# Optimization experiments

Hardware: AMD Instinct MI355X
Metric: run time of the kernel (lower is better)

Reference implementation:

```python
import jax, jax.numpy as jnp
import numpy as np

B, S, D, H = 4, 2048, 512, 8
HD = D // H  # head dim = 64


def setup_inputs() -> dict:
    key = jax.random.key(0)
    ks = jax.random.split(key, 7)
    s = 0.02
    return {
        "X": jax.random.normal(ks[0], (B, S, D), dtype=jnp.float32),
        "Y": jax.random.normal(ks[1], (B, S, D), dtype=jnp.float32),
        "Z": jax.random.normal(ks[2], (B, S, D), dtype=jnp.float32),
        # weights stored as [in, out] (torch Linear weight transposed)
        "Wq": jax.random.normal(ks[3], (D, D), dtype=jnp.float32) * s,
        "Wk": jax.random.normal(ks[4], (D, D), dtype=jnp.float32) * s,
        "Wv": jax.random.normal(ks[5], (D, D), dtype=jnp.float32) * s,  # dead in original forward
        "Wo": jax.random.normal(ks[6], (D, D), dtype=jnp.float32) * s,
    }


def _split_heads(t):
    # [B, S, D] -> [B, H, S, HD]
    return t.reshape(B, S, H, HD).transpose(0, 2, 1, 3)


def reference(X, Y, Z, Wq, Wk, Wv, Wo):
    q = _split_heads(X @ Wq)
    k = _split_heads(Y @ Wk)
    # NOTE: original module (faithfully) uses W_o for the value projection; W_v is unused.
    v = _split_heads(Z @ Wo)
    scores = jnp.einsum("bhqd,bhkd->bhqk", q, k) / jnp.sqrt(jnp.float32(HD))
    # sigmoid(s) > 0.5  <=>  s > 0 (sigmoid strictly monotone); keep score else 0
    scores = jnp.where(scores > 0, scores, jnp.float32(0))
    attn = jax.nn.softmax(scores, axis=-1)
    out = jnp.einsum("bhqk,bhkd->bhqd", attn, v)  # dropout inactive at eval
    out = out.transpose(0, 2, 1, 3).reshape(B, S, D)  # merge heads
    return out @ Wo
```

## Files before the change

kernel.cpp:

```cpp
#include <hip/hip_runtime.h>
#include <math.h>

#define S_LEN 2048
#define DIM   512
#define M_TOT 8192
#define NCH   (S_LEN / 64)

typedef __attribute__((ext_vector_type(8))) short bf16x8;
typedef __attribute__((ext_vector_type(4))) short bf16x4;
typedef __attribute__((ext_vector_type(4))) float f32x4;
typedef __attribute__((ext_vector_type(16))) float f32x16;

#define MFMA(a, b, c)   __builtin_amdgcn_mfma_f32_16x16x32_bf16((a), (b), (c), 0, 0, 0)
#define MFMA32(a, b, c) __builtin_amdgcn_mfma_f32_32x32x16_bf16((a), (b), (c), 0, 0, 0)

#define QSCALE 0.18033688011112042f

__device__ __forceinline__ short f2b(float x) {
    union { float f; unsigned u; } v; v.f = x;
    unsigned r = v.u + 0x7FFFu + ((v.u >> 16) & 1u);
    return (short)(r >> 16);
}

__device__ __forceinline__ unsigned cvtpk(float a, float b) {
    unsigned r;
    asm("v_cvt_pk_bf16_f32 %0, %1, %2" : "=v"(r) : "v"(a), "v"(b));
    return r;
}

__device__ __forceinline__ bf16x8 cvt8(float4 lo, float4 hi) {
    union { unsigned u[4]; bf16x8 v; } o;
    o.u[0] = cvtpk(lo.x, lo.y);
    o.u[1] = cvtpk(lo.z, lo.w);
    o.u[2] = cvtpk(hi.x, hi.y);
    o.u[3] = cvtpk(hi.z, hi.w);
    return o.v;
}

__device__ __forceinline__ float fast_exp2(float x) {
#if __has_builtin(__builtin_amdgcn_exp2f)
    return __builtin_amdgcn_exp2f(x);
#else
    return __expf(x * 0.693147180559945f);
#endif
}

__global__ __launch_bounds__(256) void prep_wt(const float* Wq, const float* Wk, const float* Wo,
                                               short* Wtq, short* Wtk, short* Wto) {
    const int zi = blockIdx.z;
    const float* W = zi == 0 ? Wq : zi == 1 ? Wk : Wo;
    short*      Wt = zi == 0 ? Wtq : zi == 1 ? Wtk : Wto;
    const float sc = zi == 0 ? QSCALE : 1.0f;
    __shared__ short Ts[64 * 72];
    const int t = threadIdx.x;
    const int k0 = blockIdx.x * 64, n0 = blockIdx.y * 64;
    #pragma unroll
    for (int it = 0; it < 4; ++it) {
        const int r = (t >> 4) + 16 * it;
        const int cq = t & 15;
        float4 v = *(const float4*)&W[(size_t)(k0 + r) * DIM + n0 + cq * 4];
        Ts[(4 * cq + 0) * 72 + r] = f2b(v.x * sc);
        Ts[(4 * cq + 1) * 72 + r] = f2b(v.y * sc);
        Ts[(4 * cq + 2) * 72 + r] = f2b(v.z * sc);
        Ts[(4 * cq + 3) * 72 + r] = f2b(v.w * sc);
    }
    __syncthreads();
    #pragma unroll
    for (int it = 0; it < 2; ++it) {
        const int n = (t >> 3) + 32 * it;
        const int sg = t & 7;
        *(bf16x8*)&Wt[(size_t)(n0 + n) * DIM + k0 + sg * 8] = *(const bf16x8*)&Ts[n * 72 + sg * 8];
    }
}

__global__ __launch_bounds__(256) void proj_gemm(const float* __restrict__ X,
                                                 const float* __restrict__ Y,
                                                 const float* __restrict__ Z,
                                                 const short* __restrict__ Wtq,
                                                 const short* __restrict__ Wtk,
                                                 const short* __restrict__ Wto,
                                                 short* __restrict__ Qb,
                                                 short* __restrict__ Kb,
                                                 short* __restrict__ Vt) {
    const int zi = blockIdx.z;
    const float* A  = zi == 0 ? X : zi == 1 ? Y : Z;
    const short* Bw = zi == 0 ? Wtq : zi == 1 ? Wtk : Wto;

    __shared__ short As[2][128 * 40];
    __shared__ short Bs[2][128 * 40];
    const int tid = threadIdx.x;
    const int w = tid >> 6, ln = tid & 63, l15 = ln & 15, quad = ln >> 4;
    const int m0 = blockIdx.x * 128, n0 = blockIdx.y * 128;
    const int wm = (w & 1) * 64, wn = (w >> 1) * 64;

    const int r0 = tid >> 2, r1 = r0 + 64;
    const int sg = tid & 3;
    const float* ap0 = A  + (size_t)(m0 + r0) * DIM + sg * 8;
    const float* ap1 = A  + (size_t)(m0 + r1) * DIM + sg * 8;
    const short* bp0 = Bw + (size_t)(n0 + r0) * DIM + sg * 8;
    const short* bp1 = Bw + (size_t)(n0 + r1) * DIM + sg * 8;

    float4 a0l, a0h, a1l, a1h;
    bf16x8 b0, b1;

    a0l = *(const float4*)ap0; a0h = *(const float4*)(ap0 + 4);
    a1l = *(const float4*)ap1; a1h = *(const float4*)(ap1 + 4);
    b0 = *(const bf16x8*)bp0;  b1 = *(const bf16x8*)bp1;
    *(bf16x8*)&As[0][r0 * 40 + sg * 8] = cvt8(a0l, a0h);
    *(bf16x8*)&As[0][r1 * 40 + sg * 8] = cvt8(a1l, a1h);
    *(bf16x8*)&Bs[0][r0 * 40 + sg * 8] = b0;
    *(bf16x8*)&Bs[0][r1 * 40 + sg * 8] = b1;
    a0l = *(const float4*)(ap0 + 32); a0h = *(const float4*)(ap0 + 36);
    a1l = *(const float4*)(ap1 + 32); a1h = *(const float4*)(ap1 + 36);
    b0 = *(const bf16x8*)(bp0 + 32);  b1 = *(const bf16x8*)(bp1 + 32);
    __syncthreads();

    f32x4 acc[4][4] = {};

    for (int k0 = 0; k0 < DIM; k0 += 32) {
        const int cur = (k0 >> 5) & 1;
        if (k0 + 32 < DIM) {
            *(bf16x8*)&As[cur ^ 1][r0 * 40 + sg * 8] = cvt8(a0l, a0h);
            *(bf16x8*)&As[cur ^ 1][r1 * 40 + sg * 8] = cvt8(a1l, a1h);
            *(bf16x8*)&Bs[cur ^ 1][r0 * 40 + sg * 8] = b0;
            *(bf16x8*)&Bs[cur ^ 1][r1 * 40 + sg * 8] = b1;
        }
        if (k0 + 64 < DIM) {
            const int kn = k0 + 64;
            a0l = *(const float4*)(ap0 + kn); a0h = *(const float4*)(ap0 + kn + 4);
            a1l = *(const float4*)(ap1 + kn); a1h = *(const float4*)(ap1 + kn + 4);
            b0 = *(const bf16x8*)(bp0 + kn);  b1 = *(const bf16x8*)(bp1 + kn);
        }

        bf16x8 af[4], bf[4];
        #pragma unroll
        for (int mf = 0; mf < 4; ++mf) af[mf] = *(const bf16x8*)&As[cur][(wm + 16 * mf + l15) * 40 + quad * 8];
        #pragma unroll
        for (int nf = 0; nf < 4; ++nf) bf[nf] = *(const bf16x8*)&Bs[cur][(wn + 16 * nf + l15) * 40 + quad * 8];
        #pragma unroll
        for (int mf = 0; mf < 4; ++mf)
            #pragma unroll
            for (int nf = 0; nf < 4; ++nf)
                acc[mf][nf] = MFMA(af[mf], bf[nf], acc[mf][nf]);
        __syncthreads();
    }

    if (zi < 2) {
        short* C = zi == 0 ? Qb : Kb;
        #pragma unroll
        for (int mf = 0; mf < 4; ++mf)
            #pragma unroll
            for (int nf = 0; nf < 4; ++nf)
                #pragma unroll
                for (int r = 0; r < 4; ++r)
                    C[(size_t)(m0 + wm + 16 * mf + 4 * quad + r) * DIM + n0 + wn + 16 * nf + l15] =
                        f2b(acc[mf][nf][r]);
    } else {
        #pragma unroll
        for (int mf = 0; mf < 4; ++mf)
            #pragma unroll
            for (int nf = 0; nf < 4; ++nf) {
                const int col = n0 + wn + 16 * nf + l15;
                const int h = col >> 6, hd = col & 63;
                const int row0_ = m0 + wm + 16 * mf + 4 * quad;
                const int bb = row0_ >> 11, s0 = row0_ & 2047;
                bf16x4 o = { f2b(acc[mf][nf][0]), f2b(acc[mf][nf][1]),
                             f2b(acc[mf][nf][2]), f2b(acc[mf][nf][3]) };
                *(bf16x4*)&Vt[((size_t)((bb * 8 + h) * 64 + hd)) * S_LEN + s0] = o;
            }
    }
}

__global__ __launch_bounds__(256) void out_gemm(const short* __restrict__ Ob,
                                                const short* __restrict__ Wto,
                                                float* __restrict__ Cout) {
    __shared__ short As[2][64 * 40];
    __shared__ short Bs[2][64 * 40];
    const int tid = threadIdx.x;
    const int w = tid >> 6, ln = tid & 63, l15 = ln & 15, quad = ln >> 4;

    const int f = blockIdx.x;
    const int swz = ((f & 7) << 7) | (f >> 3);
    const int m0 = (swz >> 3) * 64, n0 = (swz & 7) * 64;
    const int wm = (w & 1) * 32, wn = (w >> 1) * 32;

    const int row = tid >> 2;
    const int sg = tid & 3;
    const short* ap = Ob  + (size_t)(m0 + row) * DIM + sg * 8;
    const short* bp = Wto + (size_t)(n0 + row) * DIM + sg * 8;

    bf16x8 a0, b0;

    a0 = *(const bf16x8*)ap;  b0 = *(const bf16x8*)bp;
    *(bf16x8*)&As[0][row * 40 + sg * 8] = a0;
    *(bf16x8*)&Bs[0][row * 40 + sg * 8] = b0;
    a0 = *(const bf16x8*)(ap + 32);  b0 = *(const bf16x8*)(bp + 32);
    __syncthreads();

    f32x4 acc[2][2] = {};

    for (int k0 = 0; k0 < DIM; k0 += 32) {
        const int cur = (k0 >> 5) & 1;
        if (k0 + 32 < DIM) {
            *(bf16x8*)&As[cur ^ 1][row * 40 + sg * 8] = a0;
            *(bf16x8*)&Bs[cur ^ 1][row * 40 + sg * 8] = b0;
        }
        if (k0 + 64 < DIM) {
            a0 = *(const bf16x8*)(ap + k0 + 64);
            b0 = *(const bf16x8*)(bp + k0 + 64);
        }

        bf16x8 af[2], bf[2];
        #pragma unroll
        for (int mf = 0; mf < 2; ++mf) af[mf] = *(const bf16x8*)&As[cur][(wm + 16 * mf + l15) * 40 + quad * 8];
        #pragma unroll
        for (int nf = 0; nf < 2; ++nf) bf[nf] = *(const bf16x8*)&Bs[cur][(wn + 16 * nf + l15) * 40 + quad * 8];
        #pragma unroll
        for (int mf = 0; mf < 2; ++mf)
            #pragma unroll
            for (int nf = 0; nf < 2; ++nf)
                acc[mf][nf] = MFMA(af[mf], bf[nf], acc[mf][nf]);
        __syncthreads();
    }
    #pragma unroll
    for (int mf = 0; mf < 2; ++mf)
        #pragma unroll
        for (int nf = 0; nf < 2; ++nf)
            #pragma unroll
            for (int r = 0; r < 4; ++r)
                Cout[(size_t)(m0 + wm + 16 * mf + 4 * quad + r) * DIM + n0 + wn + 16 * nf + l15] =
                    acc[mf][nf][r];
}

__global__ __launch_bounds__(256) void attn_mfma(const short* __restrict__ Qb,
                                                 const short* __restrict__ Kb,
                                                 const short* __restrict__ Vtg,
                                                 short* __restrict__ Ob) {
    __shared__ short Ks[2][64 * 72];
    __shared__ short Vs[2][64 * 72];
    __shared__ float Ds[4][32];

    const int tid = threadIdx.x;
    const int w = tid >> 6, ln = tid & 63, n31 = ln & 31, hL = ln >> 5;

    const int f = blockIdx.x;
    const int swz = ((f & 7) << 6) | (f >> 3);
    const int qt0 = (swz & 15) * 128;
    const int bh  = swz >> 4;
    const int b = bh >> 3, h = bh & 7;
    const size_t tokbase = (size_t)b * S_LEN;

    const int q0w = qt0 + 32 * w;
    bf16x8 qf[4];
    #pragma unroll
    for (int dk = 0; dk < 4; ++dk)
        qf[dk] = *(const bf16x8*)&Qb[(tokbase + q0w + n31) * DIM + h * 64 + 16 * dk + 8 * hL];

    const int srow = tid >> 2, sg = tid & 3;
    const short* kbase = Kb  + (tokbase + srow) * DIM + h * 64 + sg * 16;
    const short* vbase = Vtg + ((size_t)bh * 64 + srow) * S_LEN;

    union b8split { bf16x8 v; struct { bf16x4 lo, hi; } s; };

    bf16x8 kr0, kr1;
    b8split vrA, vrB;

    f32x16 oacc[2] = {};
    f32x4 d4 = {0.f, 0.f, 0.f, 0.f};

    kr0 = *(const bf16x8*)kbase;       kr1 = *(const bf16x8*)(kbase + 8);
    vrA.v = *(const bf16x8*)(vbase + 8 * sg);
    vrB.v = *(const bf16x8*)(vbase + 32 + 8 * sg);
    *(bf16x8*)&Ks[0][srow * 72 + sg * 16]     = kr0;
    *(bf16x8*)&Ks[0][srow * 72 + sg * 16 + 8] = kr1;
    {
        short* vrow = &Vs[0][srow * 72 + 16 * sg];
        *(bf16x4*)&vrow[0]  = vrA.s.lo;  *(bf16x4*)&vrow[8]  = vrA.s.hi;
        *(bf16x4*)&vrow[4]  = vrB.s.lo;  *(bf16x4*)&vrow[12] = vrB.s.hi;
    }
    kr0 = *(const bf16x8*)(kbase + (size_t)64 * DIM);
    kr1 = *(const bf16x8*)(kbase + (size_t)64 * DIM + 8);
    vrA.v = *(const bf16x8*)(vbase + 64 + 8 * sg);
    vrB.v = *(const bf16x8*)(vbase + 64 + 32 + 8 * sg);
    __syncthreads();

    for (int kc = 0; kc < NCH; ++kc) {
        const int cur = kc & 1;
        if (kc + 1 < NCH) {
            *(bf16x8*)&Ks[cur ^ 1][srow * 72 + sg * 16]     = kr0;
            *(bf16x8*)&Ks[cur ^ 1][srow * 72 + sg * 16 + 8] = kr1;
            short* vrow = &Vs[cur ^ 1][srow * 72 + 16 * sg];
            *(bf16x4*)&vrow[0]  = vrA.s.lo;  *(bf16x4*)&vrow[8]  = vrA.s.hi;
            *(bf16x4*)&vrow[4]  = vrB.s.lo;  *(bf16x4*)&vrow[12] = vrB.s.hi;
        }
        if (kc + 2 < NCH) {
            const size_t ko = (size_t)(kc + 2) * 64 * DIM;
            const size_t vo = (size_t)(kc + 2) * 64;
            kr0 = *(const bf16x8*)(kbase + ko);
            kr1 = *(const bf16x8*)(kbase + ko + 8);
            vrA.v = *(const bf16x8*)(vbase + vo + 8 * sg);
            vrB.v = *(const bf16x8*)(vbase + vo + 32 + 8 * sg);
        }

        f32x16 sacc[2] = {};
        __builtin_amdgcn_s_setprio(1);
        #pragma unroll
        for (int kt = 0; kt < 2; ++kt)
            #pragma unroll
            for (int dk = 0; dk < 4; ++dk) {
                bf16x8 ka = *(const bf16x8*)&Ks[cur][(32 * kt + n31) * 72 + 16 * dk + 8 * hL];
                sacc[kt] = MFMA32(ka, qf[dk], sacc[kt]);
            }
        __builtin_amdgcn_s_setprio(0);

        unsigned cp[16];
        #pragma unroll
        for (int kt = 0; kt < 2; ++kt)
            #pragma unroll
            for (int p = 0; p < 8; ++p) {
                const float e0 = fast_exp2(fmaxf(sacc[kt][2 * p], 0.f));
                const float e1 = fast_exp2(fmaxf(sacc[kt][2 * p + 1], 0.f));
                d4[p & 3] += e0 + e1;
                cp[8 * kt + p] = cvtpk(e0, e1);
            }

        __builtin_amdgcn_s_setprio(1);
        #pragma unroll
        for (int m = 0; m < 4; ++m) {
            union { unsigned u[4]; bf16x8 v; } pu;
            pu.u[0] = cp[2 * m];     pu.u[1] = cp[2 * m + 1];
            pu.u[2] = cp[2 * m + 8]; pu.u[3] = cp[2 * m + 9];
            #pragma unroll
            for (int nt = 0; nt < 2; ++nt) {
                bf16x8 vb = *(const bf16x8*)&Vs[cur][(32 * nt + n31) * 72 + 16 * m + 8 * hL];
                oacc[nt] = MFMA32(pu.v, vb, oacc[nt]);
            }
        }
        __builtin_amdgcn_s_setprio(0);
        __syncthreads();
    }

    float dtot = (d4[0] + d4[1]) + (d4[2] + d4[3]);
    dtot += __shfl_xor(dtot, 32);
    const float dinv = 1.0f / dtot;
    if (ln < 32) Ds[w][n31] = dinv;
    __syncthreads();
    f32x4 dv[4];
    #pragma unroll
    for (int g = 0; g < 4; ++g)
        dv[g] = *(const f32x4*)&Ds[w][8 * g + 4 * hL];

    #pragma unroll
    for (int nt = 0; nt < 2; ++nt)
        #pragma unroll
        for (int r = 0; r < 16; ++r) {
            const int qb = 32 * w + 4 * hL + 8 * (r >> 2) + (r & 3);
            Ob[(tokbase + qt0 + qb) * DIM + h * 64 + 32 * nt + n31] =
                f2b(oacc[nt][r] * dv[r >> 2][r & 3]);
        }
}

extern "C" void kernel_launch(void* const* d_in, const int* in_sizes, int n_in,
                              void* d_out, int out_size, void* d_ws, size_t ws_size,
                              hipStream_t stream) {
    const float* X  = (const float*)d_in[0];
    const float* Y  = (const float*)d_in[1];
    const float* Z  = (const float*)d_in[2];
    const float* Wq = (const float*)d_in[3];
    const float* Wk = (const float*)d_in[4];
    const float* Wo = (const float*)d_in[6];

    char* p = (char*)d_ws;
    const size_t MD = (size_t)M_TOT * DIM;
    short* Qb  = (short*)p; p += MD * 2;
    short* Kb  = (short*)p; p += MD * 2;
    short* Vt  = (short*)p; p += MD * 2;
    short* Ob  = (short*)p; p += MD * 2;
    short* Wtq = (short*)p; p += (size_t)DIM * DIM * 2;
    short* Wtk = (short*)p; p += (size_t)DIM * DIM * 2;
    short* Wto = (short*)p; p += (size_t)DIM * DIM * 2;

    prep_wt<<<dim3(8, 8, 3), 256, 0, stream>>>(Wq, Wk, Wo, Wtq, Wtk, Wto);
    proj_gemm<<<dim3(64, 4, 3), 256, 0, stream>>>(X, Y, Z, Wtq, Wtk, Wto, Qb, Kb, Vt);
    attn_mfma<<<dim3(512), 256, 0, stream>>>(Qb, Kb, Vt, Ob);
    out_gemm<<<dim3(1024), 256, 0, stream>>>(Ob, Wto, (float*)d_out);
}
```

Measured before the change: 192.2 us.

## Rework projection GEMM to 32x32x16 MFMA with K=64 stages

The projection GEMM moves from 16x16x32 MFMA on 32-wide K slices to 32x32x16 MFMA on 64-wide K stages. Each wave now owns a 128x32 output strip. The A fragment is shared across waves and the B fragment is reused across four M fragments. Fewer K iterations mean fewer barriers, and the larger MFMA shape gives more compute per LDS read. In exchange, shared memory grows to about 72 KB per block and more global loads are held in registers, which may lower occupancy. The per-element epilogue stores to Q/K also change their coalescing pattern.

Result: slower. 199.1 us (+3.6%).

```diff
diff --git a/kernel.cpp b/kernel.cpp
--- a/kernel.cpp
+++ b/kernel.cpp
@@ -86,86 +86,87 @@
     const float* A  = zi == 0 ? X : zi == 1 ? Y : Z;
     const short* Bw = zi == 0 ? Wtq : zi == 1 ? Wtk : Wto;
 
-    __shared__ short As[2][128 * 40];
-    __shared__ short Bs[2][128 * 40];
+    __shared__ short As[2][128 * 72];
+    __shared__ short Bs[2][128 * 72];
     const int tid = threadIdx.x;
-    const int w = tid >> 6, ln = tid & 63, l15 = ln & 15, quad = ln >> 4;
+    const int w = tid >> 6, ln = tid & 63, n31 = ln & 31, hL = ln >> 5;
     const int m0 = blockIdx.x * 128, n0 = blockIdx.y * 128;
-    const int wm = (w & 1) * 64, wn = (w >> 1) * 64;
-
-    const int r0 = tid >> 2, r1 = r0 + 64;
-    const int sg = tid & 3;
-    const float* ap0 = A  + (size_t)(m0 + r0) * DIM + sg * 8;
-    const float* ap1 = A  + (size_t)(m0 + r1) * DIM + sg * 8;
-    const short* bp0 = Bw + (size_t)(n0 + r0) * DIM + sg * 8;
-    const short* bp1 = Bw + (size_t)(n0 + r1) * DIM + sg * 8;
-
-    float4 a0l, a0h, a1l, a1h;
-    bf16x8 b0, b1;
-
-    a0l = *(const float4*)ap0; a0h = *(const float4*)(ap0 + 4);
-    a1l = *(const float4*)ap1; a1h = *(const float4*)(ap1 + 4);
-    b0 = *(const bf16x8*)bp0;  b1 = *(const bf16x8*)bp1;
-    *(bf16x8*)&As[0][r0 * 40 + sg * 8] = cvt8(a0l, a0h);
-    *(bf16x8*)&As[0][r1 * 40 + sg * 8] = cvt8(a1l, a1h);
-    *(bf16x8*)&Bs[0][r0 * 40 + sg * 8] = b0;
-    *(bf16x8*)&Bs[0][r1 * 40 + sg * 8] = b1;
-    a0l = *(const float4*)(ap0 + 32); a0h = *(const float4*)(ap0 + 36);
-    a1l = *(const float4*)(ap1 + 32); a1h = *(const float4*)(ap1 + 36);
-    b0 = *(const bf16x8*)(bp0 + 32);  b1 = *(const bf16x8*)(bp1 + 32);
-    __syncthreads();
-
-    f32x4 acc[4][4] = {};
-
-    for (int k0 = 0; k0 < DIM; k0 += 32) {
-        const int cur = (k0 >> 5) & 1;
-        if (k0 + 32 < DIM) {
-            *(bf16x8*)&As[cur ^ 1][r0 * 40 + sg * 8] = cvt8(a0l, a0h);
-            *(bf16x8*)&As[cur ^ 1][r1 * 40 + sg * 8] = cvt8(a1l, a1h);
-            *(bf16x8*)&Bs[cur ^ 1][r0 * 40 + sg * 8] = b0;
-            *(bf16x8*)&Bs[cur ^ 1][r1 * 40 + sg * 8] = b1;
-        }
-        if (k0 + 64 < DIM) {
-            const int kn = k0 + 64;
-            a0l = *(const float4*)(ap0 + kn); a0h = *(const float4*)(ap0 + kn + 4);
-            a1l = *(const float4*)(ap1 + kn); a1h = *(const float4*)(ap1 + kn + 4);
-            b0 = *(const bf16x8*)(bp0 + kn);  b1 = *(const bf16x8*)(bp1 + kn);
-        }
-
-        bf16x8 af[4], bf[4];
-        #pragma unroll
-        for (int mf = 0; mf < 4; ++mf) af[mf] = *(const bf16x8*)&As[cur][(wm + 16 * mf + l15) * 40 + quad * 8];
-        #pragma unroll
-        for (int nf = 0; nf < 4; ++nf) bf[nf] = *(const bf16x8*)&Bs[cur][(wn + 16 * nf + l15) * 40 + quad * 8];
-        #pragma unroll
-        for (int mf = 0; mf < 4; ++mf)
-            #pragma unroll
-            for (int nf = 0; nf < 4; ++nf)
-                acc[mf][nf] = MFMA(af[mf], bf[nf], acc[mf][nf]);
+
+    const int srow = tid >> 1, sh = (tid & 1) * 32;
+    const float* ap = A  + (size_t)(m0 + srow) * DIM + sh;
+    const short* bp = Bw + (size_t)(n0 + srow) * DIM + sh;
+
+    float4 ar[8];
+    bf16x8 brr[4];
+
+    #pragma unroll
+    for (int i = 0; i < 8; ++i) ar[i] = *(const float4*)(ap + 4 * i);
+    #pragma unroll
+    for (int i = 0; i < 4; ++i) brr[i] = *(const bf16x8*)(bp + 8 * i);
+    #pragma unroll
+    for (int i = 0; i < 4; ++i)
+        *(bf16x8*)&As[0][srow * 72 + sh + 8 * i] = cvt8(ar[2 * i], ar[2 * i + 1]);
+    #pragma unroll
+    for (int i = 0; i < 4; ++i)
+        *(bf16x8*)&Bs[0][srow * 72 + sh + 8 * i] = brr[i];
+    #pragma unroll
+    for (int i = 0; i < 8; ++i) ar[i] = *(const float4*)(ap + 64 + 4 * i);
+    #pragma unroll
+    for (int i = 0; i < 4; ++i) brr[i] = *(const bf16x8*)(bp + 64 + 8 * i);
+    __syncthreads();
+
+    f32x16 acc[4] = {};
+
+    for (int it = 0; it < 8; ++it) {
+        const int cur = it & 1;
+        if (it + 1 < 8) {
+            #pragma unroll
+            for (int i = 0; i < 4; ++i)
+                *(bf16x8*)&As[cur ^ 1][srow * 72 + sh + 8 * i] = cvt8(ar[2 * i], ar[2 * i + 1]);
+            #pragma unroll
+            for (int i = 0; i < 4; ++i)
+                *(bf16x8*)&Bs[cur ^ 1][srow * 72 + sh + 8 * i] = brr[i];
+        }
+        if (it + 2 < 8) {
+            const int kb = 64 * (it + 2);
+            #pragma unroll
+            for (int i = 0; i < 8; ++i) ar[i] = *(const float4*)(ap + kb + 4 * i);
+            #pragma unroll
+            for (int i = 0; i < 4; ++i) brr[i] = *(const bf16x8*)(bp + kb + 8 * i);
+        }
+
+        #pragma unroll
+        for (int kf = 0; kf < 4; ++kf) {
+            bf16x8 bfr = *(const bf16x8*)&Bs[cur][(32 * w + n31) * 72 + 16 * kf + 8 * hL];
+            #pragma unroll
+            for (int mf = 0; mf < 4; ++mf) {
+                bf16x8 af = *(const bf16x8*)&As[cur][(32 * mf + n31) * 72 + 16 * kf + 8 * hL];
+                acc[mf] = MFMA32(af, bfr, acc[mf]);
+            }
+        }
         __syncthreads();
     }
 
+    const int col = n0 + 32 * w + n31;
     if (zi < 2) {
         short* C = zi == 0 ? Qb : Kb;
         #pragma unroll
         for (int mf = 0; mf < 4; ++mf)
             #pragma unroll
-            for (int nf = 0; nf < 4; ++nf)
-                #pragma unroll
-                for (int r = 0; r < 4; ++r)
-                    C[(size_t)(m0 + wm + 16 * mf + 4 * quad + r) * DIM + n0 + wn + 16 * nf + l15] =
-                        f2b(acc[mf][nf][r]);
+            for (int r = 0; r < 16; ++r) {
+                const int rowo = m0 + 32 * mf + (r & 3) + 8 * (r >> 2) + 4 * hL;
+                C[(size_t)rowo * DIM + col] = f2b(acc[mf][r]);
+            }
     } else {
+        const int h = col >> 6, hd = col & 63;
         #pragma unroll
         for (int mf = 0; mf < 4; ++mf)
             #pragma unroll
-            for (int nf = 0; nf < 4; ++nf) {
-                const int col = n0 + wn + 16 * nf + l15;
-                const int h = col >> 6, hd = col & 63;
-                const int row0_ = m0 + wm + 16 * mf + 4 * quad;
+            for (int rr = 0; rr < 4; ++rr) {
+                const int row0_ = m0 + 32 * mf + 8 * rr + 4 * hL;
                 const int bb = row0_ >> 11, s0 = row0_ & 2047;
-                bf16x4 o = { f2b(acc[mf][nf][0]), f2b(acc[mf][nf][1]),
-                             f2b(acc[mf][nf][2]), f2b(acc[mf][nf][3]) };
+                bf16x4 o = { f2b(acc[mf][4 * rr + 0]), f2b(acc[mf][4 * rr + 1]),
+                             f2b(acc[mf][4 * rr + 2]), f2b(acc[mf][4 * rr + 3]) };
                 *(bf16x4*)&Vt[((size_t)((bb * 8 + h) * 64 + hd)) * S_LEN + s0] = o;
             }
     }
```

## Double attention block to 8 waves and 256 queries to share K/V tiles

Applied to the files above, without the earlier changes.

The attention kernel now runs 512-thread blocks covering 256 query rows per (batch, head) instead of 128, with half as many blocks. Each K/V tile staged in shared memory is reused by twice as many waves, and each thread loads only one 16-byte K and V chunk per stage. The aim is less global K/V traffic per query. In exchange the grid has only 256 blocks, which may underfill the GPU's compute units, and the larger block may lower occupancy.

New measurement: 180.5 us. 1.06x faster.

```diff
diff --git a/kernel.cpp b/kernel.cpp
--- a/kernel.cpp
+++ b/kernel.cpp
@@ -232,21 +232,21 @@
                     acc[mf][nf][r];
 }
 
-__global__ __launch_bounds__(256) void attn_mfma(const short* __restrict__ Qb,
+__global__ __launch_bounds__(512) void attn_mfma(const short* __restrict__ Qb,
                                                  const short* __restrict__ Kb,
                                                  const short* __restrict__ Vtg,
                                                  short* __restrict__ Ob) {
     __shared__ short Ks[2][64 * 72];
     __shared__ short Vs[2][64 * 72];
-    __shared__ float Ds[4][32];
+    __shared__ float Ds[8][32];
 
     const int tid = threadIdx.x;
     const int w = tid >> 6, ln = tid & 63, n31 = ln & 31, hL = ln >> 5;
 
     const int f = blockIdx.x;
-    const int swz = ((f & 7) << 6) | (f >> 3);
-    const int qt0 = (swz & 15) * 128;
-    const int bh  = swz >> 4;
+    const int swz = ((f & 7) << 5) | (f >> 3);
+    const int qt0 = (swz & 7) * 256;
+    const int bh  = swz >> 3;
     const int b = bh >> 3, h = bh & 7;
     const size_t tokbase = (size_t)b * S_LEN;
 
@@ -256,50 +256,40 @@
     for (int dk = 0; dk < 4; ++dk)
         qf[dk] = *(const bf16x8*)&Qb[(tokbase + q0w + n31) * DIM + h * 64 + 16 * dk + 8 * hL];
 
-    const int srow = tid >> 2, sg = tid & 3;
-    const short* kbase = Kb  + (tokbase + srow) * DIM + h * 64 + sg * 16;
-    const short* vbase = Vtg + ((size_t)bh * 64 + srow) * S_LEN;
+    const int srow = tid >> 3, sg = tid & 7;
+    const int vm = sg & 3, vhalf = sg >> 2;
+    const short* kbase = Kb  + (tokbase + srow) * DIM + h * 64 + sg * 8;
+    const short* vbase = Vtg + ((size_t)bh * 64 + srow) * S_LEN + 32 * vhalf + 8 * vm;
+    const int kw_off = srow * 72 + sg * 8;
+    const int vw_off = srow * 72 + 16 * vm + 4 * vhalf;
 
     union b8split { bf16x8 v; struct { bf16x4 lo, hi; } s; };
 
-    bf16x8 kr0, kr1;
-    b8split vrA, vrB;
+    bf16x8 kr;
+    b8split vr;
 
     f32x16 oacc[2] = {};
     f32x4 d4 = {0.f, 0.f, 0.f, 0.f};
 
-    kr0 = *(const bf16x8*)kbase;       kr1 = *(const bf16x8*)(kbase + 8);
-    vrA.v = *(const bf16x8*)(vbase + 8 * sg);
-    vrB.v = *(const bf16x8*)(vbase + 32 + 8 * sg);
-    *(bf16x8*)&Ks[0][srow * 72 + sg * 16]     = kr0;
-    *(bf16x8*)&Ks[0][srow * 72 + sg * 16 + 8] = kr1;
-    {
-        short* vrow = &Vs[0][srow * 72 + 16 * sg];
-        *(bf16x4*)&vrow[0]  = vrA.s.lo;  *(bf16x4*)&vrow[8]  = vrA.s.hi;
-        *(bf16x4*)&vrow[4]  = vrB.s.lo;  *(bf16x4*)&vrow[12] = vrB.s.hi;
-    }
-    kr0 = *(const bf16x8*)(kbase + (size_t)64 * DIM);
-    kr1 = *(const bf16x8*)(kbase + (size_t)64 * DIM + 8);
-    vrA.v = *(const bf16x8*)(vbase + 64 + 8 * sg);
-    vrB.v = *(const bf16x8*)(vbase + 64 + 32 + 8 * sg);
+    kr   = *(const bf16x8*)kbase;
+    vr.v = *(const bf16x8*)vbase;
+    *(bf16x8*)&Ks[0][kw_off] = kr;
+    *(bf16x4*)&Vs[0][vw_off]     = vr.s.lo;
+    *(bf16x4*)&Vs[0][vw_off + 8] = vr.s.hi;
+    kr   = *(const bf16x8*)(kbase + (size_t)64 * DIM);
+    vr.v = *(const bf16x8*)(vbase + 64);
     __syncthreads();
 
     for (int kc = 0; kc < NCH; ++kc) {
         const int cur = kc & 1;
         if (kc + 1 < NCH) {
-            *(bf16x8*)&Ks[cur ^ 1][srow * 72 + sg * 16]     = kr0;
-            *(bf16x8*)&Ks[cur ^ 1][srow * 72 + sg * 16 + 8] = kr1;
-            short* vrow = &Vs[cur ^ 1][srow * 72 + 16 * sg];
-            *(bf16x4*)&vrow[0]  = vrA.s.lo;  *(bf16x4*)&vrow[8]  = vrA.s.hi;
-            *(bf16x4*)&vrow[4]  = vrB.s.lo;  *(bf16x4*)&vrow[12] = vrB.s.hi;
+            *(bf16x8*)&Ks[cur ^ 1][kw_off] = kr;
+            *(bf16x4*)&Vs[cur ^ 1][vw_off]     = vr.s.lo;
+            *(bf16x4*)&Vs[cur ^ 1][vw_off + 8] = vr.s.hi;
         }
         if (kc + 2 < NCH) {
-            const size_t ko = (size_t)(kc + 2) * 64 * DIM;
-            const size_t vo = (size_t)(kc + 2) * 64;
-            kr0 = *(const bf16x8*)(kbase + ko);
-            kr1 = *(const bf16x8*)(kbase + ko + 8);
-            vrA.v = *(const bf16x8*)(vbase + vo + 8 * sg);
-            vrB.v = *(const bf16x8*)(vbase + vo + 32 + 8 * sg);
+            kr   = *(const bf16x8*)(kbase + (size_t)(kc + 2) * 64 * DIM);
+            vr.v = *(const bf16x8*)(vbase + (size_t)(kc + 2) * 64);
         }
 
         f32x16 sacc[2] = {};
@@ -382,6 +372,6 @@
 
     prep_wt<<<dim3(8, 8, 3), 256, 0, stream>>>(Wq, Wk, Wo, Wtq, Wtk, Wto);
     proj_gemm<<<dim3(64, 4, 3), 256, 0, stream>>>(X, Y, Z, Wtq, Wtk, Wto, Qb, Kb, Vt);
-    attn_mfma<<<dim3(512), 256, 0, stream>>>(Qb, Kb, Vt, Ob);
+    attn_mfma<<<dim3(256), 512, 0, stream>>>(Qb, Kb, Vt, Ob);
     out_gemm<<<dim3(1024), 256, 0, stream>>>(Ob, Wto, (float*)d_out);
 }
```
